# Performance work log

Measured on AMD Instinct MI355X. Metric: run time of the kernel, lower is better.

The kernel has to match this reference:

```python
import jax, jax.numpy as jnp
import numpy as np

B, S, D, H, HG, W, DFF = 2, 4096, 1024, 16, 2, 128, 4096
NEG = -1e30  # stands in for -inf in the original masking (exp underflows to exactly 0)


def _chunk(x, w):
    # overlapping chunks of size 2w with hop w (tf.signal.frame equivalent)
    b, s, d = x.shape
    blocks = x.reshape(b, s // w, w, d)
    return jnp.concatenate([blocks[:, :-1], blocks[:, 1:]], axis=2)  # [b, s//w-1, 2w, d]


def _sliding_scores(q, k, w):
    # q,k: [BH, S, dh] (q pre-scaled). Returns banded scores [BH, S, 2w+1].
    bh, s, d = q.shape
    c = s // w - 1
    attn = jnp.einsum('bcxd,bcyd->bcxy', _chunk(q, w), _chunk(k, w))  # [bh,c,2w,2w]
    # pad one row then reshape: the skew trick from the source (_pad_and_transpose_last_two_dims)
    dca = jnp.pad(attn, ((0, 0), (0, 0), (0, 1), (0, 0))).reshape(bh, c, 2 * w, 2 * w + 1)
    up = jnp.concatenate([dca[:, :, :w, :w + 1], dca[:, -1:, w:, :w + 1]], axis=1)          # [bh,c+1,w,w+1]
    first = jnp.roll(dca, shift=(1, w), axis=(2, 3))[:, :1, :w, :w]                          # first-chunk lower triangle
    low = jnp.concatenate([first, dca[:, :, -(w + 1):-1, w + 1:]], axis=1)                   # [bh,c+1,w,w]
    return jnp.concatenate([low, up], axis=-1).reshape(bh, s, 2 * w + 1)


def _invalid_mask(s, w):
    # _mask_invalid_locations: mask band positions that fall outside [0, S)
    m = jnp.tril(jnp.ones((w, w + 1), jnp.float32))[::-1]
    m = jnp.pad(m, ((0, s - w), (0, w)))
    return (m + m[::-1, ::-1]) > 0  # [s, 2w+1]


def _sliding_value(p, v, w):
    # p: [BH, S, 2w+1] band probs, v: [BH, S, dh] -> [BH, S, dh]
    bh, s, kk = p.shape
    d = v.shape[-1]
    c = s // w
    cp = jnp.pad(p.reshape(bh, c, w, kk), ((0, 0), (0, 0), (0, 0), (0, w + 1)))
    # pad-and-diagonalize skew: row r shifted right by r -> aligns band with 3w value window
    cp = cp.reshape(bh, c, w * (3 * w + 2))[:, :, :-w].reshape(bh, c, w, 3 * w + 1)[:, :, :, :-1]
    pv = jnp.pad(v, ((0, 0), (w, w), (0, 0))).reshape(bh, c + 2, w, d)
    cv = jnp.concatenate([pv[:, :-2], pv[:, 1:-1], pv[:, 2:]], axis=2)  # [bh,c,3w,d]
    return jnp.einsum('bcwk,bckd->bcwd', cp, cv).reshape(bh, s, d)


def _layernorm(x, g, b):
    mu = jnp.mean(x, -1, keepdims=True)
    var = jnp.mean(jnp.square(x - mu), -1, keepdims=True)
    return (x - mu) * jax.lax.rsqrt(var + 1e-6) * g + b


def setup_inputs() -> dict:
    key = jax.random.key(0)
    ks = jax.random.split(key, 8)
    dense = lambda k, i, o: 0.02 * jax.random.normal(k, (i, o), jnp.float32)
    return {
        'x': jax.random.normal(ks[0], (B, S, D), jnp.float32),
        'mask': jnp.zeros((B, 1, 1, S), jnp.float32),
        'wq_k': dense(ks[1], D, D), 'wq_b': jnp.zeros((D,), jnp.float32),
        'wk_k': dense(ks[2], D, D), 'wk_b': jnp.zeros((D,), jnp.float32),
        'wv_k': dense(ks[3], D, D), 'wv_b': jnp.zeros((D,), jnp.float32),
        'wo_k': dense(ks[4], D, D), 'wo_b': jnp.zeros((D,), jnp.float32),
        'ffn_w1': dense(ks[5], D, DFF), 'ffn_b1': jnp.zeros((DFF,), jnp.float32),
        'ffn_w2': dense(ks[6], DFF, D), 'ffn_b2': jnp.zeros((D,), jnp.float32),
        'ln1_g': jnp.ones((D,), jnp.float32), 'ln1_b': jnp.zeros((D,), jnp.float32),
        'ln2_g': jnp.ones((D,), jnp.float32), 'ln2_b': jnp.zeros((D,), jnp.float32),
    }


def reference(x, mask, wq_k, wq_b, wk_k, wk_b, wv_k, wv_b, wo_k, wo_b,
              ffn_w1, ffn_b1, ffn_w2, ffn_b2, ln1_g, ln1_b, ln2_g, ln2_b):
    dh = D // H
    hl = H - HG
    split = lambda t: t.reshape(B, S, H, dh).transpose(0, 2, 1, 3)  # [B,H,S,dh]
    q, k, v = split(x @ wq_k + wq_b), split(x @ wk_k + wk_b), split(x @ wv_k + wv_b)
    scale = 1.0 / jnp.sqrt(jnp.float32(dh))
    # ---- local (sliding-window) heads ----
    ql = (q[:, :hl] * scale).reshape(B * hl, S, dh)
    kl = k[:, :hl].reshape(B * hl, S, dh)
    vl = v[:, :hl].reshape(B * hl, S, dh)
    scores = _sliding_scores(ql, kl, W)
    scores = jnp.where(_invalid_mask(S, W)[None], NEG, scores)
    out_l = _sliding_value(jax.nn.softmax(scores, axis=-1), vl, W).reshape(B, hl, S, dh)
    # ---- global heads (full attention, graph_mask=None branch) ----
    logits = jnp.einsum('bhqd,bhkd->bhqk', q[:, hl:], k[:, hl:]) * scale + mask * (-1000.0)
    out_g = jnp.einsum('bhqk,bhkd->bhqd', jax.nn.softmax(logits, axis=-1), v[:, hl:])
    # ---- merge heads, output proj, residual + LN, FFN (leaky_relu alpha=0.2 = tf default) ----
    attn = jnp.concatenate([out_l, out_g], axis=1).transpose(0, 2, 1, 3).reshape(B, S, D)
    out1 = _layernorm(x + attn @ wo_k + wo_b, ln1_g, ln1_b)
    h = jax.nn.leaky_relu(out1 @ ffn_w1 + ffn_b1, negative_slope=0.2)
    return _layernorm(out1 + h @ ffn_w2 + ffn_b2, ln2_g, ln2_b)
```

## Files before the change

kernel.cpp:

```cpp
#include <hip/hip_runtime.h>
#include <hip/hip_bf16.h>

typedef unsigned short u16;
typedef unsigned int u32;
typedef __attribute__((ext_vector_type(8))) short short8;
typedef __attribute__((ext_vector_type(8))) unsigned short ushort8v;
typedef __attribute__((ext_vector_type(4))) unsigned short ushort4v;
typedef __attribute__((ext_vector_type(4))) float f32x4;

static constexpr int B_ = 2, S_ = 4096, D_ = 1024, H_ = 16, HG_ = 2, W_ = 128, DFF_ = 4096;
static constexpr int HL_ = H_ - HG_;
static constexpr int M_ = B_ * S_;
static constexpr int NCH_ = 4;

static __device__ __forceinline__ u16 f2b(float f) {
    u32 u = __builtin_bit_cast(u32, f);
    u32 r = (u + 0x7fffu + ((u >> 16) & 1u)) >> 16;
    return (u16)r;
}
static __device__ __forceinline__ float b2f(u16 b) {
    return __builtin_bit_cast(float, (u32)b << 16);
}

__global__ __launch_bounds__(256) void k_f32_to_bf16(const float* __restrict__ src,
                                                     u16* __restrict__ dst, int n4) {
    int i = blockIdx.x * 256 + threadIdx.x;
    if (i >= n4) return;
    float4 v = reinterpret_cast<const float4*>(src)[i];
    ushort4v o; o[0] = f2b(v.x); o[1] = f2b(v.y); o[2] = f2b(v.z); o[3] = f2b(v.w);
    reinterpret_cast<ushort4v*>(dst)[i] = o;
}

__global__ __launch_bounds__(256) void k_transpose_bf16(const float* __restrict__ src,
                                                        u16* __restrict__ dst,
                                                        int K, int N, int ro) {
    __shared__ float tile[32][33];
    const int tx = threadIdx.x & 31, ty = threadIdx.x >> 5;
    const int bx = blockIdx.x, by = blockIdx.y;
#pragma unroll
    for (int jj = 0; jj < 4; ++jj) {
        int kk = by * 32 + ty + jj * 8;
        int nn = bx * 32 + tx;
        tile[ty + jj * 8][tx] = src[(size_t)kk * N + nn];
    }
    __syncthreads();
#pragma unroll
    for (int jj = 0; jj < 4; ++jj) {
        int nn = bx * 32 + ty + jj * 8;
        int kk = by * 32 + tx;
        dst[(size_t)(ro + nn) * K + kk] = f2b(tile[tx][ty + jj * 8]);
    }
}

__global__ __launch_bounds__(256) void k_transpose3(const float* __restrict__ a,
                                                    const float* __restrict__ b,
                                                    const float* __restrict__ c,
                                                    u16* __restrict__ dst) {
    __shared__ float tile[32][33];
    const float* src = blockIdx.z == 0 ? a : (blockIdx.z == 1 ? b : c);
    const int ro = blockIdx.z * 1024;
    const int tx = threadIdx.x & 31, ty = threadIdx.x >> 5;
    const int bx = blockIdx.x, by = blockIdx.y;
#pragma unroll
    for (int jj = 0; jj < 4; ++jj) {
        int kk = by * 32 + ty + jj * 8;
        int nn = bx * 32 + tx;
        tile[ty + jj * 8][tx] = src[(size_t)kk * 1024 + nn];
    }
    __syncthreads();
#pragma unroll
    for (int jj = 0; jj < 4; ++jj) {
        int nn = bx * 32 + ty + jj * 8;
        int kk = by * 32 + tx;
        dst[(size_t)(ro + nn) * 1024 + kk] = f2b(tile[tx][ty + jj * 8]);
    }
}

__global__ __launch_bounds__(256) void k_transpose_v(const u16* __restrict__ qkv,
                                                     u16* __restrict__ vT) {
    __shared__ u16 tile[32][33];
    const int tx = threadIdx.x & 31, ty = threadIdx.x >> 5;
    const int s0 = blockIdx.x * 32;
    const int d0 = blockIdx.y * 32;
    const int bh = blockIdx.z;
    const int b = bh >> 4, h = bh & 15;
#pragma unroll
    for (int jj = 0; jj < 4; ++jj) {
        int srow = s0 + ty + jj * 8;
        tile[ty + jj * 8][tx] = qkv[(size_t)(b * S_ + srow) * 3072 + 2048 + h * 64 + d0 + tx];
    }
    __syncthreads();
#pragma unroll
    for (int jj = 0; jj < 4; ++jj) {
        int d = d0 + ty + jj * 8;
        vT[(size_t)((b * H_ + h) * 64 + d) * S_ + s0 + tx] = tile[tx][ty + jj * 8];
    }
}

__global__ void k_pack_bias3(const float* __restrict__ a, const float* __restrict__ b,
                             const float* __restrict__ c, float* __restrict__ dst) {
    int i = blockIdx.x * 256 + threadIdx.x;
    if (i >= 3072) return;
    dst[i] = i < 1024 ? a[i] : (i < 2048 ? b[i - 1024] : c[i - 2048]);
}

#define GLDS16(gp, lp) __builtin_amdgcn_global_load_lds( \
    (const __attribute__((address_space(1))) void*)(gp),  \
    (__attribute__((address_space(3))) void*)(lp), 16, 0, 0)

template <bool LEAKY, bool OUTF, bool OUTB>
__global__ __launch_bounds__(256) void k_gemm(const u16* __restrict__ A, const u16* __restrict__ Bt,
                                              const float* __restrict__ bias,
                                              float* __restrict__ Cf, u16* __restrict__ Cb,
                                              int M, int N, int K) {
    __shared__ __align__(16) u16 lA[128 * 64];
    __shared__ __align__(16) u16 lB[128 * 64];
    const int tid = threadIdx.x;
    const int lane = tid & 63, wave = tid >> 6;
    const int wr = wave >> 1, wc = wave & 1;
    const int m0 = blockIdx.x * 128, n0 = blockIdx.y * 128;

    f32x4 acc[4][4];
#pragma unroll
    for (int i = 0; i < 4; ++i)
#pragma unroll
        for (int j = 0; j < 4; ++j)
#pragma unroll
            for (int e = 0; e < 4; ++e) acc[i][j][e] = 0.f;

    const int srow = tid >> 3;
    const int sgc = (tid & 7) ^ (srow & 7);
    const int c = lane & 15, g4 = lane >> 4;

    const u16* gA = A + (size_t)(m0 + srow) * K + sgc * 8;
    const u16* gB = Bt + (size_t)(n0 + srow) * K + sgc * 8;

    const char* lAc = reinterpret_cast<const char*>(lA);
    const char* lBc = reinterpret_cast<const char*>(lB);

    for (int k0 = 0; k0 < K; k0 += 64) {
        __syncthreads();
#pragma unroll
        for (int j = 0; j < 4; ++j) {
            GLDS16(gA + k0 + (size_t)j * 32 * K, lA + j * 2048 + wave * 512);
            GLDS16(gB + k0 + (size_t)j * 32 * K, lB + j * 2048 + wave * 512);
        }
        __syncthreads();

#pragma unroll
        for (int ks = 0; ks < 2; ++ks) {
            short8 af[4], bfr[4];
#pragma unroll
            for (int mi = 0; mi < 4; ++mi) {
                const int r = wr * 64 + mi * 16 + c;
                const int gl = (ks * 4 + g4) ^ (c & 7);
                af[mi] = *reinterpret_cast<const short8*>(lAc + r * 128 + gl * 16);
            }
#pragma unroll
            for (int ni = 0; ni < 4; ++ni) {
                const int r = wc * 64 + ni * 16 + c;
                const int gl = (ks * 4 + g4) ^ (c & 7);
                bfr[ni] = *reinterpret_cast<const short8*>(lBc + r * 128 + gl * 16);
            }
            __builtin_amdgcn_s_setprio(1);
#pragma unroll
            for (int mi = 0; mi < 4; ++mi)
#pragma unroll
                for (int ni = 0; ni < 4; ++ni)
                    acc[mi][ni] = __builtin_amdgcn_mfma_f32_16x16x32_bf16(af[mi], bfr[ni], acc[mi][ni], 0, 0, 0);
            __builtin_amdgcn_s_setprio(0);
        }
    }

#pragma unroll
    for (int mi = 0; mi < 4; ++mi) {
        const int rowb = m0 + wr * 64 + mi * 16 + (lane >> 4) * 4;
#pragma unroll
        for (int ni = 0; ni < 4; ++ni) {
            const int col = n0 + wc * 64 + ni * 16 + (lane & 15);
            const float bs = bias[col];
#pragma unroll
            for (int j = 0; j < 4; ++j) {
                float v = acc[mi][ni][j] + bs;
                if (LEAKY) v = v > 0.f ? v : 0.2f * v;
                const size_t idx = (size_t)(rowb + j) * N + col;
                if (OUTF) Cf[idx] = v;
                if (OUTB) Cb[idx] = f2b(v);
            }
        }
    }
}

__global__ __launch_bounds__(256) void k_attn_local(const u16* __restrict__ qkv,
                                                    const u16* __restrict__ vT,
                                                    u16* __restrict__ out) {
    __shared__ __align__(16) u16 Kl[64][72];
    __shared__ __align__(16) u16 Vl[64][72];
    __shared__ __align__(16) u16 Pl[4][1024];
    const int tid = threadIdx.x, lane = tid & 63, wave = tid >> 6;
    const int c = lane & 15, g = lane >> 4;
    const int b = blockIdx.z, h = blockIdx.y;
    const int qbl = blockIdx.x;
    const int qb = ((qbl & 7) << 3) | (qbl >> 3);
    const int q0 = qb * 64;
    const int qrow = q0 + wave * 16 + c;

    short8 qf[2];
    {
        const u16* qp = qkv + (size_t)(b * S_ + qrow) * 3072 + h * 64 + g * 8;
        qf[0] = *reinterpret_cast<const short8*>(qp);
        qf[1] = *reinterpret_cast<const short8*>(qp + 32);
    }

    f32x4 acc[4];
#pragma unroll
    for (int dt = 0; dt < 4; ++dt)
#pragma unroll
        for (int j = 0; j < 4; ++j) acc[dt][j] = 0.f;
    float mrow = -1e30f, lrow = 0.f;

    const int t_lo = max(0, q0 - W_) >> 6;
    const int t_hi = min(S_ - 1, q0 + 63 + W_) >> 6;
    u16* pw = Pl[wave];

    const int r0 = tid >> 3, cb0 = (tid & 7) * 8, r1 = r0 + 32;
    const u16* kbase = qkv + (size_t)b * S_ * 3072 + 1024 + h * 64 + cb0;
    const u16* vbase = vT + ((size_t)(b * H_ + h) * 64) * S_ + cb0;
    ushort8v ka0 = *reinterpret_cast<const ushort8v*>(kbase + (size_t)(t_lo * 64 + r0) * 3072);
    ushort8v ka1 = *reinterpret_cast<const ushort8v*>(kbase + (size_t)(t_lo * 64 + r1) * 3072);
    ushort8v va0 = *reinterpret_cast<const ushort8v*>(vbase + (size_t)r0 * S_ + t_lo * 64);
    ushort8v va1 = *reinterpret_cast<const ushort8v*>(vbase + (size_t)r1 * S_ + t_lo * 64);

    for (int t = t_lo; t <= t_hi; ++t) {
        __syncthreads();
        *reinterpret_cast<ushort8v*>(&Kl[r0][cb0]) = ka0;
        *reinterpret_cast<ushort8v*>(&Kl[r1][cb0]) = ka1;
        *reinterpret_cast<ushort8v*>(&Vl[r0][cb0]) = va0;
        *reinterpret_cast<ushort8v*>(&Vl[r1][cb0]) = va1;
        if (t < t_hi) {
            ka0 = *reinterpret_cast<const ushort8v*>(kbase + (size_t)((t + 1) * 64 + r0) * 3072);
            ka1 = *reinterpret_cast<const ushort8v*>(kbase + (size_t)((t + 1) * 64 + r1) * 3072);
            va0 = *reinterpret_cast<const ushort8v*>(vbase + (size_t)r0 * S_ + (t + 1) * 64);
            va1 = *reinterpret_cast<const ushort8v*>(vbase + (size_t)r1 * S_ + (t + 1) * 64);
        }
        __syncthreads();

        f32x4 s[4];
#pragma unroll
        for (int nt = 0; nt < 4; ++nt)
#pragma unroll
            for (int j = 0; j < 4; ++j) s[nt][j] = 0.f;
        __builtin_amdgcn_s_setprio(1);
#pragma unroll
        for (int kc = 0; kc < 2; ++kc) {
#pragma unroll
            for (int nt = 0; nt < 4; ++nt) {
                short8 kf = *reinterpret_cast<const short8*>(&Kl[nt * 16 + c][kc * 32 + g * 8]);
                s[nt] = __builtin_amdgcn_mfma_f32_16x16x32_bf16(kf, qf[kc], s[nt], 0, 0, 0);
            }
        }
        __builtin_amdgcn_s_setprio(0);

        float p[4][4];
        float tmax = -1e30f;
#pragma unroll
        for (int nt = 0; nt < 4; ++nt)
#pragma unroll
            for (int j = 0; j < 4; ++j) {
                float sv = s[nt][j] * 0.125f;
                int key = t * 64 + nt * 16 + 4 * g + j;
                bool val = (key >= qrow - W_) && (key <= qrow + W_);
                sv = val ? sv : -1e30f;
                p[nt][j] = sv;
                tmax = fmaxf(tmax, sv);
            }
        tmax = fmaxf(tmax, __shfl_xor(tmax, 16));
        tmax = fmaxf(tmax, __shfl_xor(tmax, 32));
        float mnew = fmaxf(mrow, tmax);
        float fac = __expf(mrow - mnew);
        mrow = mnew;
        float psum = 0.f;
#pragma unroll
        for (int nt = 0; nt < 4; ++nt)
#pragma unroll
            for (int j = 0; j < 4; ++j) {
                p[nt][j] = __expf(p[nt][j] - mnew);
                psum += p[nt][j];
            }
        lrow = lrow * fac + psum;
#pragma unroll
        for (int dt = 0; dt < 4; ++dt)
#pragma unroll
            for (int j = 0; j < 4; ++j) acc[dt][j] *= fac;

#pragma unroll
        for (int nt = 0; nt < 4; ++nt)
#pragma unroll
            for (int jp = 0; jp < 2; ++jp) {
                u32 pk = (u32)f2b(p[nt][2 * jp]) | ((u32)f2b(p[nt][2 * jp + 1]) << 16);
                int byteoff = (c << 7) + ((nt * 32 + 8 * g + 4 * jp) ^ ((c & 7) << 4));
                *reinterpret_cast<u32*>(reinterpret_cast<char*>(pw) + byteoff) = pk;
            }
        asm volatile("s_waitcnt lgkmcnt(0)" ::: "memory");

        __builtin_amdgcn_s_setprio(1);
#pragma unroll
        for (int h2 = 0; h2 < 2; ++h2) {
            int rb = (c << 7) + ((h2 * 64 + g * 16) ^ ((c & 7) << 4));
            short8 pa = *reinterpret_cast<const short8*>(reinterpret_cast<char*>(pw) + rb);
#pragma unroll
            for (int dt = 0; dt < 4; ++dt) {
                short8 vf = *reinterpret_cast<const short8*>(&Vl[dt * 16 + c][h2 * 32 + g * 8]);
                acc[dt] = __builtin_amdgcn_mfma_f32_16x16x32_bf16(vf, pa, acc[dt], 0, 0, 0);
            }
        }
        __builtin_amdgcn_s_setprio(0);
    }

    float lfull = lrow + __shfl_xor(lrow, 16);
    lfull += __shfl_xor(lfull, 32);
    const float rinv = 1.0f / lfull;

#pragma unroll
    for (int dt = 0; dt < 4; ++dt) {
        u32 w0 = (u32)f2b(acc[dt][0] * rinv) | ((u32)f2b(acc[dt][1] * rinv) << 16);
        u32 w1 = (u32)f2b(acc[dt][2] * rinv) | ((u32)f2b(acc[dt][3] * rinv) << 16);
        uint2 wv; wv.x = w0; wv.y = w1;
        *reinterpret_cast<uint2*>(out + (size_t)(b * S_ + qrow) * 1024 + h * 64 + dt * 16 + 4 * g) = wv;
    }
}

__global__ __launch_bounds__(256) void k_attn_global_part(const u16* __restrict__ qkv,
                                                          const u16* __restrict__ vT,
                                                          const float* __restrict__ mask,
                                                          float* __restrict__ po,
                                                          float* __restrict__ ml) {
    __shared__ __align__(16) u16 Kl[64][72];
    __shared__ __align__(16) u16 Vl[64][72];
    __shared__ __align__(16) u16 Pl[4][1024];
    __shared__ float maskl[64];
    const int tid = threadIdx.x, lane = tid & 63, wave = tid >> 6;
    const int c = lane & 15, g = lane >> 4;
    const int b = blockIdx.z;
    const int hh = blockIdx.x >> 2, ch = blockIdx.x & 3;
    const int h = HL_ + hh;
    const int qb = blockIdx.y;
    const int q0 = qb * 64;
    const int qrow = q0 + wave * 16 + c;

    short8 qf[2];
    {
        const u16* qp = qkv + (size_t)(b * S_ + qrow) * 3072 + h * 64 + g * 8;
        qf[0] = *reinterpret_cast<const short8*>(qp);
        qf[1] = *reinterpret_cast<const short8*>(qp + 32);
    }

    f32x4 acc[4];
#pragma unroll
    for (int dt = 0; dt < 4; ++dt)
#pragma unroll
        for (int j = 0; j < 4; ++j) acc[dt][j] = 0.f;
    float mrow = -1e30f, lrow = 0.f;
    u16* pw = Pl[wave];

    const int t_lo = ch * (S_ / 64 / NCH_), t_hi = t_lo + (S_ / 64 / NCH_) - 1;

    const int r0 = tid >> 3, cb0 = (tid & 7) * 8, r1 = r0 + 32;
    const u16* kbase = qkv + (size_t)b * S_ * 3072 + 1024 + h * 64 + cb0;
    const u16* vbase = vT + ((size_t)(b * H_ + h) * 64) * S_ + cb0;
    ushort8v ka0 = *reinterpret_cast<const ushort8v*>(kbase + (size_t)(t_lo * 64 + r0) * 3072);
    ushort8v ka1 = *reinterpret_cast<const ushort8v*>(kbase + (size_t)(t_lo * 64 + r1) * 3072);
    ushort8v va0 = *reinterpret_cast<const ushort8v*>(vbase + (size_t)r0 * S_ + t_lo * 64);
    ushort8v va1 = *reinterpret_cast<const ushort8v*>(vbase + (size_t)r1 * S_ + t_lo * 64);
    float mk = (tid < 64) ? mask[(size_t)b * S_ + t_lo * 64 + tid] : 0.f;

    for (int t = t_lo; t <= t_hi; ++t) {
        __syncthreads();
        *reinterpret_cast<ushort8v*>(&Kl[r0][cb0]) = ka0;
        *reinterpret_cast<ushort8v*>(&Kl[r1][cb0]) = ka1;
        *reinterpret_cast<ushort8v*>(&Vl[r0][cb0]) = va0;
        *reinterpret_cast<ushort8v*>(&Vl[r1][cb0]) = va1;
        if (tid < 64) maskl[tid] = mk * (-1000.0f);
        if (t < t_hi) {
            ka0 = *reinterpret_cast<const ushort8v*>(kbase + (size_t)((t + 1) * 64 + r0) * 3072);
            ka1 = *reinterpret_cast<const ushort8v*>(kbase + (size_t)((t + 1) * 64 + r1) * 3072);
            va0 = *reinterpret_cast<const ushort8v*>(vbase + (size_t)r0 * S_ + (t + 1) * 64);
            va1 = *reinterpret_cast<const ushort8v*>(vbase + (size_t)r1 * S_ + (t + 1) * 64);
            if (tid < 64) mk = mask[(size_t)b * S_ + (t + 1) * 64 + tid];
        }
        __syncthreads();

        f32x4 s[4];
#pragma unroll
        for (int nt = 0; nt < 4; ++nt)
#pragma unroll
            for (int j = 0; j < 4; ++j) s[nt][j] = 0.f;
        __builtin_amdgcn_s_setprio(1);
#pragma unroll
        for (int kc = 0; kc < 2; ++kc) {
#pragma unroll
            for (int nt = 0; nt < 4; ++nt) {
                short8 kf = *reinterpret_cast<const short8*>(&Kl[nt * 16 + c][kc * 32 + g * 8]);
                s[nt] = __builtin_amdgcn_mfma_f32_16x16x32_bf16(kf, qf[kc], s[nt], 0, 0, 0);
            }
        }
        __builtin_amdgcn_s_setprio(0);

        float p[4][4];
        float tmax = -1e30f;
#pragma unroll
        for (int nt = 0; nt < 4; ++nt)
#pragma unroll
            for (int j = 0; j < 4; ++j) {
                float sv = s[nt][j] * 0.125f + maskl[nt * 16 + 4 * g + j];
                p[nt][j] = sv;
                tmax = fmaxf(tmax, sv);
            }
        tmax = fmaxf(tmax, __shfl_xor(tmax, 16));
        tmax = fmaxf(tmax, __shfl_xor(tmax, 32));
        float mnew = fmaxf(mrow, tmax);
        float fac = __expf(mrow - mnew);
        mrow = mnew;
        float psum = 0.f;
#pragma unroll
        for (int nt = 0; nt < 4; ++nt)
#pragma unroll
            for (int j = 0; j < 4; ++j) {
                p[nt][j] = __expf(p[nt][j] - mnew);
                psum += p[nt][j];
            }
        lrow = lrow * fac + psum;
#pragma unroll
        for (int dt = 0; dt < 4; ++dt)
#pragma unroll
            for (int j = 0; j < 4; ++j) acc[dt][j] *= fac;

#pragma unroll
        for (int nt = 0; nt < 4; ++nt)
#pragma unroll
            for (int jp = 0; jp < 2; ++jp) {
                u32 pk = (u32)f2b(p[nt][2 * jp]) | ((u32)f2b(p[nt][2 * jp + 1]) << 16);
                int byteoff = (c << 7) + ((nt * 32 + 8 * g + 4 * jp) ^ ((c & 7) << 4));
                *reinterpret_cast<u32*>(reinterpret_cast<char*>(pw) + byteoff) = pk;
            }
        asm volatile("s_waitcnt lgkmcnt(0)" ::: "memory");

        __builtin_amdgcn_s_setprio(1);
#pragma unroll
        for (int h2 = 0; h2 < 2; ++h2) {
            int rb = (c << 7) + ((h2 * 64 + g * 16) ^ ((c & 7) << 4));
            short8 pa = *reinterpret_cast<const short8*>(reinterpret_cast<char*>(pw) + rb);
#pragma unroll
            for (int dt = 0; dt < 4; ++dt) {
                short8 vf = *reinterpret_cast<const short8*>(&Vl[dt * 16 + c][h2 * 32 + g * 8]);
                acc[dt] = __builtin_amdgcn_mfma_f32_16x16x32_bf16(vf, pa, acc[dt], 0, 0, 0);
            }
        }
        __builtin_amdgcn_s_setprio(0);
    }

    float lfull = lrow + __shfl_xor(lrow, 16);
    lfull += __shfl_xor(lfull, 32);

    float* po_blk = po + ((((size_t)(b * HG_ + hh) * NCH_ + ch) * (S_ / 64) + qb) * 4096);
    const int ql = wave * 16 + c;
#pragma unroll
    for (int dt = 0; dt < 4; ++dt)
        *reinterpret_cast<f32x4*>(po_blk + ql * 64 + dt * 16 + 4 * g) = acc[dt];
    if (g == 0) {
        size_t mb = (((size_t)(b * HG_ + hh) * NCH_ + ch) * S_ + q0 + ql) * 2;
        ml[mb] = mrow;
        ml[mb + 1] = lfull;
    }
}

__global__ __launch_bounds__(256) void k_attn_merge(const float* __restrict__ po,
                                                    const float* __restrict__ ml,
                                                    u16* __restrict__ out) {
    const int qb = blockIdx.x, hh = blockIdx.y, b = blockIdx.z;
    const int t = threadIdx.x;
    const int ql = t >> 2, d0 = (t & 3) * 16;
    const int q = qb * 64 + ql;

    float mv[NCH_], lv[NCH_];
    float M = -1e30f;
#pragma unroll
    for (int ch = 0; ch < NCH_; ++ch) {
        size_t mb = (((size_t)(b * HG_ + hh) * NCH_ + ch) * S_ + q) * 2;
        mv[ch] = ml[mb];
        lv[ch] = ml[mb + 1];
        M = fmaxf(M, mv[ch]);
    }
    float wch[NCH_], L = 0.f;
#pragma unroll
    for (int ch = 0; ch < NCH_; ++ch) {
        wch[ch] = __expf(mv[ch] - M);
        L += wch[ch] * lv[ch];
    }
    const float rL = 1.0f / L;

    float o[16];
#pragma unroll
    for (int i = 0; i < 16; ++i) o[i] = 0.f;
#pragma unroll
    for (int ch = 0; ch < NCH_; ++ch) {
        const float* pb = po + ((((size_t)(b * HG_ + hh) * NCH_ + ch) * (S_ / 64) + qb) * 4096) + ql * 64 + d0;
        const float w = wch[ch];
#pragma unroll
        for (int i = 0; i < 4; ++i) {
            float4 v = reinterpret_cast<const float4*>(pb)[i];
            o[4 * i + 0] += w * v.x; o[4 * i + 1] += w * v.y;
            o[4 * i + 2] += w * v.z; o[4 * i + 3] += w * v.w;
        }
    }
    ushort8v r0, r1;
#pragma unroll
    for (int i = 0; i < 8; ++i) { r0[i] = f2b(o[i] * rL); r1[i] = f2b(o[8 + i] * rL); }
    u16* op = out + (size_t)(b * S_ + q) * 1024 + (HL_ + hh) * 64 + d0;
    *reinterpret_cast<ushort8v*>(op) = r0;
    *reinterpret_cast<ushort8v*>(op + 8) = r1;
}

template <bool BASEF>
__global__ __launch_bounds__(256) void k_ln(const float* __restrict__ basef, const u16* __restrict__ baseb,
                                            const u16* __restrict__ delta,
                                            const float* __restrict__ g, const float* __restrict__ bt,
                                            float* __restrict__ outf, u16* __restrict__ outb) {
    __shared__ float red[8];
    const int row = blockIdx.x, tid = threadIdx.x;
    const int lane = tid & 63, wave = tid >> 6;
    float x0, x1, x2, x3;
    if (BASEF) {
        float4 xb = reinterpret_cast<const float4*>(basef + (size_t)row * 1024)[tid];
        x0 = xb.x; x1 = xb.y; x2 = xb.z; x3 = xb.w;
    } else {
        ushort4v xb = reinterpret_cast<const ushort4v*>(baseb + (size_t)row * 1024)[tid];
        x0 = b2f(xb[0]); x1 = b2f(xb[1]); x2 = b2f(xb[2]); x3 = b2f(xb[3]);
    }
    ushort4v xd = reinterpret_cast<const ushort4v*>(delta + (size_t)row * 1024)[tid];
    x0 += b2f(xd[0]); x1 += b2f(xd[1]); x2 += b2f(xd[2]); x3 += b2f(xd[3]);
    float s = x0 + x1 + x2 + x3;
#pragma unroll
    for (int off = 32; off >= 1; off >>= 1) s += __shfl_xor(s, off);
    if (lane == 0) red[wave] = s;
    __syncthreads();
    float mu = (red[0] + red[1] + red[2] + red[3]) * (1.f / 1024.f);
    float d0 = x0 - mu, d1 = x1 - mu, d2 = x2 - mu, d3 = x3 - mu;
    float s2 = d0 * d0 + d1 * d1 + d2 * d2 + d3 * d3;
#pragma unroll
    for (int off = 32; off >= 1; off >>= 1) s2 += __shfl_xor(s2, off);
    if (lane == 0) red[4 + wave] = s2;
    __syncthreads();
    float var = (red[4] + red[5] + red[6] + red[7]) * (1.f / 1024.f);
    float rs = rsqrtf(var + 1e-6f);
    float4 gv = reinterpret_cast<const float4*>(g)[tid];
    float4 bv = reinterpret_cast<const float4*>(bt)[tid];
    float o0 = d0 * rs * gv.x + bv.x;
    float o1 = d1 * rs * gv.y + bv.y;
    float o2 = d2 * rs * gv.z + bv.z;
    float o3 = d3 * rs * gv.w + bv.w;
    if (outf) {
        float4 ov; ov.x = o0; ov.y = o1; ov.z = o2; ov.w = o3;
        reinterpret_cast<float4*>(outf + (size_t)row * 1024)[tid] = ov;
    }
    if (outb) {
        ushort4v ob; ob[0] = f2b(o0); ob[1] = f2b(o1); ob[2] = f2b(o2); ob[3] = f2b(o3);
        reinterpret_cast<ushort4v*>(outb + (size_t)row * 1024)[tid] = ob;
    }
}

extern "C" void kernel_launch(void* const* d_in, const int* in_sizes, int n_in,
                              void* d_out, int out_size, void* d_ws, size_t ws_size,
                              hipStream_t stream) {
    const float* x    = (const float*)d_in[0];
    const float* mask = (const float*)d_in[1];
    const float* wq   = (const float*)d_in[2];
    const float* wq_b = (const float*)d_in[3];
    const float* wk   = (const float*)d_in[4];
    const float* wk_b = (const float*)d_in[5];
    const float* wv   = (const float*)d_in[6];
    const float* wv_b = (const float*)d_in[7];
    const float* wo   = (const float*)d_in[8];
    const float* wo_b = (const float*)d_in[9];
    const float* w1   = (const float*)d_in[10];
    const float* b1   = (const float*)d_in[11];
    const float* w2   = (const float*)d_in[12];
    const float* b2   = (const float*)d_in[13];
    const float* ln1g = (const float*)d_in[14];
    const float* ln1b = (const float*)d_in[15];
    const float* ln2g = (const float*)d_in[16];
    const float* ln2b = (const float*)d_in[17];
    float* out = (float*)d_out;

    char* ws = (char*)d_ws;
    const size_t MB = 1024ull * 1024ull;
    u16*   qkv_b  = (u16*)(ws + 0);
    u16*   h_b    = (u16*)(ws + 0);
    u16*   vTb    = (u16*)(ws + 64 * MB);
    u16*   ybuf_b = (u16*)(ws + 64 * MB);
    u16*   ffn2_b = (u16*)(ws + 64 * MB);
    float* po     = (float*)(ws + 96 * MB);
    float* ml     = (float*)(ws + 113 * MB);
    u16*   xb     = (u16*)(ws + 128 * MB);
    u16*   attn_b = (u16*)(ws + 128 * MB);
    u16*   out1_b = (u16*)(ws + 128 * MB);
    u16*   wT     = (u16*)(ws + 144 * MB);
    float* bias3  = (float*)(ws + 152 * MB);

    const dim3 tb(256);

    k_f32_to_bf16<<<(M_ * D_ / 4 + 255) / 256, tb, 0, stream>>>(x, xb, M_ * D_ / 4);
    k_transpose3<<<dim3(32, 32, 3), tb, 0, stream>>>(wq, wk, wv, wT);
    k_pack_bias3<<<12, tb, 0, stream>>>(wq_b, wk_b, wv_b, bias3);
    k_gemm<false, false, true><<<dim3(M_ / 128, 3072 / 128), tb, 0, stream>>>(
        xb, wT, bias3, nullptr, qkv_b, M_, 3072, 1024);
    k_transpose_v<<<dim3(S_ / 32, 2, B_ * H_), tb, 0, stream>>>(qkv_b, vTb);
    k_attn_local<<<dim3(S_ / 64, HL_, B_), tb, 0, stream>>>(qkv_b, vTb, attn_b);
    k_attn_global_part<<<dim3(HG_ * NCH_, S_ / 64, B_), tb, 0, stream>>>(qkv_b, vTb, mask, po, ml);
    k_attn_merge<<<dim3(S_ / 64, HG_, B_), tb, 0, stream>>>(po, ml, attn_b);
    k_transpose_bf16<<<dim3(32, 32), tb, 0, stream>>>(wo, wT, 1024, 1024, 0);
    k_gemm<false, false, true><<<dim3(M_ / 128, 1024 / 128), tb, 0, stream>>>(
        attn_b, wT, wo_b, nullptr, ybuf_b, M_, 1024, 1024);
    k_ln<true><<<M_, tb, 0, stream>>>(x, nullptr, ybuf_b, ln1g, ln1b, nullptr, out1_b);
    k_transpose_bf16<<<dim3(128, 32), tb, 0, stream>>>(w1, wT, 1024, 4096, 0);
    k_gemm<true, false, true><<<dim3(M_ / 128, 4096 / 128), tb, 0, stream>>>(
        out1_b, wT, b1, nullptr, h_b, M_, 4096, 1024);
    k_transpose_bf16<<<dim3(32, 128), tb, 0, stream>>>(w2, wT, 4096, 1024, 0);
    k_gemm<false, false, true><<<dim3(M_ / 128, 1024 / 128), tb, 0, stream>>>(
        h_b, wT, b2, nullptr, ffn2_b, M_, 1024, 4096);
    k_ln<false><<<M_, tb, 0, stream>>>(nullptr, out1_b, ffn2_b, ln2g, ln2b, out, nullptr);
}
```

Measured before the change: 374.5 us.

## Remap GEMM blocks per XCD and double local-attention query tile to 128

The GEMM now remaps its linear block index so that consecutive tiles land on the same XCD. The goal is better L2 reuse of the A and B tiles across the chiplets. The local sliding-window attention kernel moves from 64 to 128 query rows per block using 512 threads, so each K/V tile staged in shared memory is shared by 8 waves instead of 4, and the per-thread staging load drops to one row. This cuts redundant K/V loads but uses more registers and LDS per block, and the blocks are fewer and larger. The qb swizzle now covers only 32 query blocks, and the unseen loop body must handle the wider range of key tiles correctly.

```diff
diff --git a/kernel.cpp b/kernel.cpp
--- a/kernel.cpp
+++ b/kernel.cpp
@@ -118,7 +118,14 @@
     const int tid = threadIdx.x;
     const int lane = tid & 63, wave = tid >> 6;
     const int wr = wave >> 1, wc = wave & 1;
-    const int m0 = blockIdx.x * 128, n0 = blockIdx.y * 128;
+
+    const int GX = gridDim.x;
+    const int nwg = GX * gridDim.y;
+    const int lin = blockIdx.y * GX + blockIdx.x;
+    const int qq = nwg >> 3, rm = nwg & 7;
+    const int xcd = lin & 7, idx = lin >> 3;
+    const int wg = (xcd < rm ? xcd * (qq + 1) : rm * (qq + 1) + (xcd - rm) * qq) + idx;
+    const int m0 = (wg % GX) * 128, n0 = (wg / GX) * 128;
 
     f32x4 acc[4][4];
 #pragma unroll
@@ -183,26 +190,26 @@
             for (int j = 0; j < 4; ++j) {
                 float v = acc[mi][ni][j] + bs;
                 if (LEAKY) v = v > 0.f ? v : 0.2f * v;
-                const size_t idx = (size_t)(rowb + j) * N + col;
-                if (OUTF) Cf[idx] = v;
-                if (OUTB) Cb[idx] = f2b(v);
-            }
-        }
-    }
-}
-
-__global__ __launch_bounds__(256) void k_attn_local(const u16* __restrict__ qkv,
+                const size_t idx2 = (size_t)(rowb + j) * N + col;
+                if (OUTF) Cf[idx2] = v;
+                if (OUTB) Cb[idx2] = f2b(v);
+            }
+        }
+    }
+}
+
+__global__ __launch_bounds__(512) void k_attn_local(const u16* __restrict__ qkv,
                                                     const u16* __restrict__ vT,
                                                     u16* __restrict__ out) {
     __shared__ __align__(16) u16 Kl[64][72];
     __shared__ __align__(16) u16 Vl[64][72];
-    __shared__ __align__(16) u16 Pl[4][1024];
+    __shared__ __align__(16) u16 Pl[8][1024];
     const int tid = threadIdx.x, lane = tid & 63, wave = tid >> 6;
     const int c = lane & 15, g = lane >> 4;
     const int b = blockIdx.z, h = blockIdx.y;
     const int qbl = blockIdx.x;
-    const int qb = ((qbl & 7) << 3) | (qbl >> 3);
-    const int q0 = qb * 64;
+    const int qb = ((qbl & 7) << 2) | (qbl >> 3);
+    const int q0 = qb * 128;
     const int qrow = q0 + wave * 16 + c;
 
     short8 qf[2];
@@ -220,28 +227,24 @@
     float mrow = -1e30f, lrow = 0.f;
 
     const int t_lo = max(0, q0 - W_) >> 6;
-    const int t_hi = min(S_ - 1, q0 + 63 + W_) >> 6;
+    const int t_hi = min(S_ - 1, q0 + 127 + W_) >> 6;
     u16* pw = Pl[wave];
 
-    const int r0 = tid >> 3, cb0 = (tid & 7) * 8, r1 = r0 + 32;
+    const int r0 = tid >> 3, cb0 = (tid & 7) * 8;
     const u16* kbase = qkv + (size_t)b * S_ * 3072 + 1024 + h * 64 + cb0;
-    const u16* vbase = vT + ((size_t)(b * H_ + h) * 64) * S_ + cb0;
-    ushort8v ka0 = *reinterpret_cast<const ushort8v*>(kbase + (size_t)(t_lo * 64 + r0) * 3072);
-    ushort8v ka1 = *reinterpret_cast<const ushort8v*>(kbase + (size_t)(t_lo * 64 + r1) * 3072);
-    ushort8v va0 = *reinterpret_cast<const ushort8v*>(vbase + (size_t)r0 * S_ + t_lo * 64);
-    ushort8v va1 = *reinterpret_cast<const ushort8v*>(vbase + (size_t)r1 * S_ + t_lo * 64);
+    const u16* vbase = vT + ((size_t)(b * H_ + h) * 64 + r0) * S_ + cb0 - cb0 + cb0;
+    const u16* vrow = vT + ((size_t)(b * H_ + h) * 64 + r0) * S_;
+    ushort8v ka = *reinterpret_cast<const ushort8v*>(kbase + (size_t)(t_lo * 64 + r0) * 3072);
+    ushort8v va = *reinterpret_cast<const ushort8v*>(vrow + t_lo * 64 + cb0);
+    (void)vbase;
 
     for (int t = t_lo; t <= t_hi; ++t) {
         __syncthreads();
-        *reinterpret_cast<ushort8v*>(&Kl[r0][cb0]) = ka0;
-        *reinterpret_cast<ushort8v*>(&Kl[r1][cb0]) = ka1;
-        *reinterpret_cast<ushort8v*>(&Vl[r0][cb0]) = va0;
-        *reinterpret_cast<ushort8v*>(&Vl[r1][cb0]) = va1;
+        *reinterpret_cast<ushort8v*>(&Kl[r0][cb0]) = ka;
+        *reinterpret_cast<ushort8v*>(&Vl[r0][cb0]) = va;
         if (t < t_hi) {
-            ka0 = *reinterpret_cast<const ushort8v*>(kbase + (size_t)((t + 1) * 64 + r0) * 3072);
-            ka1 = *reinterpret_cast<const ushort8v*>(kbase + (size_t)((t + 1) * 64 + r1) * 3072);
-            va0 = *reinterpret_cast<const ushort8v*>(vbase + (size_t)r0 * S_ + (t + 1) * 64);
-            va1 = *reinterpret_cast<const ushort8v*>(vbase + (size_t)r1 * S_ + (t + 1) * 64);
+            ka = *reinterpret_cast<const ushort8v*>(kbase + (size_t)((t + 1) * 64 + r0) * 3072);
+            va = *reinterpret_cast<const ushort8v*>(vrow + (t + 1) * 64 + cb0);
         }
         __syncthreads();
 
@@ -615,7 +618,7 @@
     k_gemm<false, false, true><<<dim3(M_ / 128, 3072 / 128), tb, 0, stream>>>(
         xb, wT, bias3, nullptr, qkv_b, M_, 3072, 1024);
     k_transpose_v<<<dim3(S_ / 32, 2, B_ * H_), tb, 0, stream>>>(qkv_b, vTb);
-    k_attn_local<<<dim3(S_ / 64, HL_, B_), tb, 0, stream>>>(qkv_b, vTb, attn_b);
+    k_attn_local<<<dim3(S_ / 128, HL_, B_), dim3(512), 0, stream>>>(qkv_b, vTb, attn_b);
     k_attn_global_part<<<dim3(HG_ * NCH_, S_ / 64, B_), tb, 0, stream>>>(qkv_b, vTb, mask, po, ml);
     k_attn_merge<<<dim3(S_ / 64, HG_, B_), tb, 0, stream>>>(po, ml, attn_b);
     k_transpose_bf16<<<dim3(32, 32), tb, 0, stream>>>(wo, wT, 1024, 1024, 0);
```

After: 416.8 us. 1.11x slower.
